# Kernel tuning notes

Measured on AMD Instinct MI355X. Metric: run time of the kernel, lower is better.

Reference implementation:

```python
import jax, jax.numpy as jnp
import numpy as np

T = 4096
C = 2048
N_FEAT = 2048
NEG = -1e30  # finite stand-in for -inf so fully-masked (padding) rows stay NaN-free


def setup_inputs() -> dict:
    key = jax.random.key(0)
    kx, kw, kb = jax.random.split(key, 3)
    x = jax.random.normal(kx, (T, C), dtype=jnp.float32)
    # Dense(features=3*n_feat): kernel (C, 3*n_feat), bias (3*n_feat,)
    W = jax.random.normal(kw, (C, 3 * N_FEAT), dtype=jnp.float32) * (1.0 / np.sqrt(C))
    b = jax.random.normal(kb, (3 * N_FEAT,), dtype=jnp.float32) * 0.01
    n_padd = 128
    return {"x": x, "W": W, "b": b, "n_padd": n_padd}


def reference(x, W, b, n_padd):
    T_, _ = x.shape
    qkv = x @ W + b                      # (T, 3*n_feat)
    q, k, v = jnp.split(qkv, 3, axis=1)  # each (T, n_feat)
    scale = 1.0 / jnp.sqrt(jnp.float32(q.shape[1]))
    att = (q @ k.T) * scale              # (T, T)
    rows = jnp.arange(T_)[:, None]
    cols = jnp.arange(T_)[None, :]
    # causal AND both row/col past the left padding
    mask = (cols <= rows) & (cols >= n_padd) & (rows >= n_padd)
    att = jnp.where(mask, att, NEG)
    p = jax.nn.softmax(att, axis=1)      # stable row softmax
    # kernel only stores rows >= n_padd; padding rows are zero
    p = jnp.where(rows >= n_padd, p, 0.0)
    y = p @ v                            # (T, n_feat)
    return y
```

## Files before the change

kernel.cpp:

```cpp
#include <hip/hip_runtime.h>
#include <cstdint>


#define T_DIM 4096
#define C_DIM 2048
#define NF    2048
#define N3    6144
#define NEGV  (-1e30f)

typedef __bf16 bf16x8 __attribute__((ext_vector_type(8)));
typedef __bf16 bf16x4 __attribute__((ext_vector_type(4)));
typedef float  f32x4  __attribute__((ext_vector_type(4)));

#define FENCE() asm volatile("" ::: "memory")
#define BARRIER() do { FENCE(); __builtin_amdgcn_s_barrier(); FENCE(); } while (0)

__device__ __forceinline__ void async_cp16(const void* g, void* l) {
    __builtin_amdgcn_global_load_lds(
        reinterpret_cast<const __attribute__((address_space(1))) unsigned int*>(
            reinterpret_cast<uintptr_t>(g)),
        reinterpret_cast<__attribute__((address_space(3))) unsigned int*>(
            reinterpret_cast<uintptr_t>(l)),
        16, 0, 0);
}

__device__ __forceinline__ void gemm_loop(const __bf16* A, const __bf16* B,
                                          int lda, int ldb, int m0, int n0,
                                          int kiters, __bf16* As, __bf16* Bs,
                                          f32x4 (&acc)[4][4]) {
    if (kiters <= 0) return;
    const int t    = threadIdx.x;
    const int wv   = t >> 6;
    const int lane = t & 63;
    const int srow = t >> 3;
    const int scol = (((t & 7) ^ (srow & 7)) << 3);
    const int wm   = (wv >> 1) << 6;
    const int wn   = (wv & 1) << 6;
    const int lrow = lane & 15;
    const int kq   = lane >> 4;
    const int swz  = lrow & 7;
    const int rc0  = ((kq ^ swz) << 3);
    const int rc1  = (((kq | 4) ^ swz) << 3);

    const __bf16* ga = A + (size_t)(m0 + srow) * lda + scol;
    const __bf16* gb = B + (size_t)(n0 + srow) * ldb + scol;

    auto stage = [&](int kk, int s) {
#pragma unroll
        for (int i = 0; i < 4; ++i) {
            async_cp16(ga + kk * 64 + (size_t)(32 * i) * lda,
                       &As[s * 8192 + i * 2048 + wv * 512]);
            async_cp16(gb + kk * 64 + (size_t)(32 * i) * ldb,
                       &Bs[s * 8192 + i * 2048 + wv * 512]);
        }
    };
    auto loadF = [&](const __bf16* Ab, const __bf16* Bb, int rc,
                     bf16x8 (&af)[4], bf16x8 (&bfr)[4]) {
#pragma unroll
        for (int mi = 0; mi < 4; ++mi)
            af[mi] = *(const bf16x8*)&Ab[(wm + mi * 16 + lrow) * 64 + rc];
#pragma unroll
        for (int ni = 0; ni < 4; ++ni)
            bfr[ni] = *(const bf16x8*)&Bb[(wn + ni * 16 + lrow) * 64 + rc];
    };
    auto mfma16 = [&](bf16x8 (&af)[4], bf16x8 (&bfr)[4]) {
        __builtin_amdgcn_s_setprio(1);
#pragma unroll
        for (int mi = 0; mi < 4; ++mi)
#pragma unroll
            for (int ni = 0; ni < 4; ++ni)
                acc[mi][ni] = __builtin_amdgcn_mfma_f32_16x16x32_bf16(
                    af[mi], bfr[ni], acc[mi][ni], 0, 0, 0);
        __builtin_amdgcn_s_setprio(0);
    };

    bf16x8 af[4], bfr[4];

    stage(0, 0);
    asm volatile("s_waitcnt vmcnt(0)" ::: "memory");
    BARRIER();

    for (int kk = 0; kk < kiters; ++kk) {
        const int b = kk & 1;
        const __bf16* Ab = &As[b * 8192];
        const __bf16* Bb = &Bs[b * 8192];
        const bool pf = (kk + 1 < kiters);
        if (pf) stage(kk + 1, b ^ 1);
        loadF(Ab, Bb, rc0, af, bfr);
        mfma16(af, bfr);
        loadF(Ab, Bb, rc1, af, bfr);
        mfma16(af, bfr);
        asm volatile("s_waitcnt vmcnt(0)" ::: "memory");
        BARRIER();
    }
}

__global__ void prep_kernel(const float* __restrict__ x,
                            __bf16* __restrict__ xb,
                            const float* __restrict__ W,
                            __bf16* __restrict__ Wt) {
    if (blockIdx.x < 2048) {
        const int n4 = (T_DIM * C_DIM) / 4;
        const int stride = 2048 * 256;
        for (int i = blockIdx.x * 256 + threadIdx.x; i < n4; i += stride) {
            float4 v = ((const float4*)x)[i];
            bf16x4 o;
            o[0] = (__bf16)v.x; o[1] = (__bf16)v.y;
            o[2] = (__bf16)v.z; o[3] = (__bf16)v.w;
            ((bf16x4*)xb)[i] = o;
        }
        return;
    }
    __shared__ float tile[32][33];
    const int tb = blockIdx.x - 2048;
    const int bx = (tb % (N3 / 32)) * 32;
    const int by = (tb / (N3 / 32)) * 32;
    const int tx = threadIdx.x & 31, ty = threadIdx.x >> 5;
#pragma unroll
    for (int i = 0; i < 32; i += 8)
        tile[ty + i][tx] = W[(size_t)(by + ty + i) * N3 + bx + tx];
    __syncthreads();
#pragma unroll
    for (int i = 0; i < 32; i += 8)
        Wt[(size_t)(bx + ty + i) * C_DIM + by + tx] = (__bf16)tile[tx][ty + i];
}

#define EPILOG_SETUP()                                     \
    const int t = threadIdx.x, wv = t >> 6, lane = t & 63; \
    const int wm = (wv >> 1) << 6, wn = (wv & 1) << 6;     \
    const int rq = (lane >> 4) << 2, cn = lane & 15

__global__ void __launch_bounds__(768)
qkv_gemm_kernel(const __bf16* __restrict__ xb, const __bf16* __restrict__ Wt,
                const float* __restrict__ bias, __bf16* __restrict__ qb,
                __bf16* __restrict__ kb, __bf16* __restrict__ vT) {
    __shared__ __bf16 As[2][256 * 64];
    __shared__ __bf16 Bs[2][384 * 64];

    const int t    = threadIdx.x;
    const int wv   = t >> 6;
    const int lane = t & 63;
    const int srow = t >> 3;
    const int scol = (((t & 7) ^ (srow & 7)) << 3);
    const int m0   = blockIdx.x * 256;
    const int n0   = blockIdx.y * 384;
    const int wmo  = (wv / 6) * 128;
    const int wno  = (wv % 6) * 64;
    const int lrow = lane & 15;
    const int kq   = lane >> 4;
    const int swz  = lrow & 7;
    const int rc0  = ((kq ^ swz) << 3);
    const int rc1  = (((kq | 4) ^ swz) << 3);

    const __bf16* ga = xb + (size_t)(m0 + srow) * C_DIM + scol;
    const __bf16* gb = Wt + (size_t)(n0 + srow) * C_DIM + scol;

    f32x4 acc[8][4] = {};

    auto stageA = [&](int kt, int s) {
        const __bf16* a = ga + kt * 64;
        async_cp16(a, &As[s][wv * 512]);
        async_cp16(a + (size_t)96 * C_DIM, &As[s][6144 + wv * 512]);
        if (wv < 8)
            async_cp16(a + (size_t)192 * C_DIM, &As[s][12288 + wv * 512]);
    };
    auto stageB2 = [&](int kt, int s, int h) {
        const __bf16* b2 = gb + kt * 64 + (size_t)(192 * h) * C_DIM;
        async_cp16(b2, &Bs[s][h * 12288 + wv * 512]);
        async_cp16(b2 + (size_t)96 * C_DIM, &Bs[s][h * 12288 + 6144 + wv * 512]);
    };
    auto loadA4 = [&](const __bf16* Ab, int mh, int rc, bf16x8 (&af)[4]) {
#pragma unroll
        for (int mi = 0; mi < 4; ++mi)
            af[mi] = *(const bf16x8*)
                &Ab[(wmo + mh * 64 + mi * 16 + lrow) * 64 + rc];
    };
    auto loadB4 = [&](const __bf16* Bb, int rc, bf16x8 (&bfr)[4]) {
#pragma unroll
        for (int ni = 0; ni < 4; ++ni)
            bfr[ni] = *(const bf16x8*)&Bb[(wno + ni * 16 + lrow) * 64 + rc];
    };
    auto mfma16 = [&](bf16x8 (&af)[4], bf16x8 (&bfr)[4], int mh) {
        __builtin_amdgcn_s_setprio(1);
#pragma unroll
        for (int mi = 0; mi < 4; ++mi)
#pragma unroll
            for (int ni = 0; ni < 4; ++ni)
                acc[mh * 4 + mi][ni] = __builtin_amdgcn_mfma_f32_16x16x32_bf16(
                    af[mi], bfr[ni], acc[mh * 4 + mi][ni], 0, 0, 0);
        __builtin_amdgcn_s_setprio(0);
    };

    bf16x8 af[4], bfr[4];
    constexpr int KT = C_DIM / 64;

    stageA(0, 0); stageB2(0, 0, 0); stageB2(0, 0, 1);
    asm volatile("s_waitcnt vmcnt(0)" ::: "memory");
    BARRIER();

    for (int kt = 0; kt < KT; ++kt) {
        const int b = kt & 1;
        const __bf16* Ab = As[b];
        const __bf16* Bb = Bs[b];
        const bool pf = (kt + 1 < KT);
        loadB4(Bb, rc0, bfr);
        loadA4(Ab, 0, rc0, af);
        if (pf) stageA(kt + 1, b ^ 1);
        BARRIER();
        mfma16(af, bfr, 0);
        BARRIER();
        loadA4(Ab, 1, rc0, af);
        if (pf) stageB2(kt + 1, b ^ 1, 0);
        BARRIER();
        mfma16(af, bfr, 1);
        BARRIER();
        loadB4(Bb, rc1, bfr);
        loadA4(Ab, 0, rc1, af);
        if (pf) stageB2(kt + 1, b ^ 1, 1);
        BARRIER();
        mfma16(af, bfr, 0);
        BARRIER();
        loadA4(Ab, 1, rc1, af);
        BARRIER();
        mfma16(af, bfr, 1);
        if (pf) asm volatile("s_waitcnt vmcnt(0)" ::: "memory");
        BARRIER();
    }

    const int rq = (lane >> 4) << 2, cn = lane & 15;
#pragma unroll
    for (int mi = 0; mi < 8; ++mi)
#pragma unroll
        for (int ni = 0; ni < 4; ++ni) {
            int col = n0 + wno + ni * 16 + cn;
            float bv = bias[col];
            if (col >= 2 * NF) {
                bf16x4 o;
#pragma unroll
                for (int r = 0; r < 4; ++r) o[r] = (__bf16)(acc[mi][ni][r] + bv);
                int row = m0 + wmo + mi * 16 + rq;
                *(bf16x4*)&vT[(size_t)(col - 2 * NF) * T_DIM + row] = o;
            } else {
#pragma unroll
                for (int r = 0; r < 4; ++r) {
                    int row = m0 + wmo + mi * 16 + rq + r;
                    float val = acc[mi][ni][r] + bv;
                    if (col < NF)
                        qb[(size_t)row * NF + col] = (__bf16)val;
                    else
                        kb[(size_t)row * NF + (col - NF)] = (__bf16)val;
                }
            }
        }
}

__global__ void __launch_bounds__(256)
sc_gemm_kernel(const __bf16* __restrict__ qb, const __bf16* __restrict__ kb,
               __bf16* __restrict__ S, const int* __restrict__ npadd_p) {
    int i = blockIdx.x;
    int mt = (int)((sqrtf(8.0f * (float)i + 1.0f) - 1.0f) * 0.5f);
    while ((mt + 1) * (mt + 2) / 2 <= i) ++mt;
    while (mt * (mt + 1) / 2 > i) --mt;
    int nt = i - mt * (mt + 1) / 2;
    const int m0 = mt * 128, n0 = nt * 128;
    const int npadd = *npadd_p;
    if (m0 + 128 <= npadd || n0 + 128 <= npadd) return;

    __shared__ __bf16 As[2 * 128 * 64];
    __shared__ __bf16 Bs[2 * 128 * 64];
    f32x4 acc[4][4] = {};
    gemm_loop(qb, kb, NF, NF, m0, n0, NF / 64, As, Bs, acc);

    const float scale = 0.022097086912079608f;
    EPILOG_SETUP();
#pragma unroll
    for (int mi = 0; mi < 4; ++mi)
#pragma unroll
        for (int ni = 0; ni < 4; ++ni) {
            int j = n0 + wn + ni * 16 + cn;
#pragma unroll
            for (int r = 0; r < 4; ++r) {
                int row = m0 + wm + mi * 16 + rq + r;
                S[(size_t)row * T_DIM + j] = (__bf16)(acc[mi][ni][r] * scale);
            }
        }
}

__global__ void __launch_bounds__(256)
softmax_kernel(const __bf16* __restrict__ S, __bf16* __restrict__ P,
               const int* __restrict__ npadd_p) {
    const int wv = threadIdx.x >> 6, lane = threadIdx.x & 63;
    const int row = blockIdx.x * 4 + wv;
    const int npadd = *npadd_p;
    __bf16* prow = P + (size_t)row * T_DIM;

    if (row < npadd) {
        bf16x8 z = {};
#pragma unroll
        for (int c = 0; c < 8; ++c) ((bf16x8*)prow)[c * 64 + lane] = z;
        return;
    }

    const __bf16* srow = S + (size_t)row * T_DIM;
    float vals[64];
    float mx = NEGV;
#pragma unroll
    for (int c = 0; c < 8; ++c) {
        if (c * 512 > row) {
#pragma unroll
            for (int e = 0; e < 8; ++e) vals[c * 8 + e] = NEGV;
            continue;
        }
        int j0 = c * 512 + lane * 8;
        bf16x8 v = ((const bf16x8*)srow)[c * 64 + lane];
#pragma unroll
        for (int e = 0; e < 8; ++e) {
            float f = (j0 + e >= npadd && j0 + e <= row) ? (float)v[e] : NEGV;
            vals[c * 8 + e] = f;
            mx = fmaxf(mx, f);
        }
    }
#pragma unroll
    for (int o = 32; o > 0; o >>= 1) mx = fmaxf(mx, __shfl_xor(mx, o));

    float sm = 0.f;
#pragma unroll
    for (int k = 0; k < 64; ++k) {
        vals[k] = exp2f((vals[k] - mx) * 1.4426950408889634f);
        sm += vals[k];
    }
#pragma unroll
    for (int o = 32; o > 0; o >>= 1) sm += __shfl_xor(sm, o);
    float inv = 1.0f / sm;

#pragma unroll
    for (int c = 0; c < 8; ++c) {
        bf16x8 o;
#pragma unroll
        for (int e = 0; e < 8; ++e) o[e] = (__bf16)(vals[c * 8 + e] * inv);
        ((bf16x8*)prow)[c * 64 + lane] = o;
    }
}

__global__ void __launch_bounds__(256)
pv_gemm_kernel(const __bf16* __restrict__ P, const __bf16* __restrict__ vT,
               float* __restrict__ out, const int* __restrict__ npadd_p) {
    const int idx = blockIdx.x;
    const int kskip = *npadd_p >> 6;
    int mt, nt, start, iters;
    bool atomic_out;
    if (idx < 256) {
        mt = idx & 15; nt = idx >> 4;
        int kt = (mt + 1) * 2 - kskip; if (kt < 0) kt = 0;
        start = kskip; iters = kt; atomic_out = false;
    } else {
        int j = idx - 256;
        mt = 16 + (j & 15); nt = (j >> 4) & 15;
        int half = j >> 8;
        int kt = (mt + 1) * 2 - kskip; if (kt < 0) kt = 0;
        int h0 = (kt + 1) >> 1;
        start = kskip + (half ? h0 : 0);
        iters = half ? kt - h0 : h0;
        atomic_out = true;
    }
    const int m0 = mt * 128, n0 = nt * 128;

    __shared__ __bf16 As[2 * 128 * 64];
    __shared__ __bf16 Bs[2 * 128 * 64];
    f32x4 acc[4][4] = {};
    gemm_loop(P + (size_t)start * 64, vT + (size_t)start * 64,
              T_DIM, T_DIM, m0, n0, iters, As, Bs, acc);

    EPILOG_SETUP();
#pragma unroll
    for (int mi = 0; mi < 4; ++mi)
#pragma unroll
        for (int ni = 0; ni < 4; ++ni) {
            int col = n0 + wn + ni * 16 + cn;
#pragma unroll
            for (int r = 0; r < 4; ++r) {
                int row = m0 + wm + mi * 16 + rq + r;
                float* p = &out[(size_t)row * NF + col];
                if (atomic_out) unsafeAtomicAdd(p, acc[mi][ni][r]);
                else            *p = acc[mi][ni][r];
            }
        }
}

extern "C" void kernel_launch(void* const* d_in, const int* in_sizes, int n_in,
                              void* d_out, int out_size, void* d_ws,
                              size_t ws_size, hipStream_t stream) {
    const float* x = (const float*)d_in[0];
    const float* W = (const float*)d_in[1];
    const float* b = (const float*)d_in[2];
    const int* npadd = (const int*)d_in[3];
    float* out = (float*)d_out;

    char* ws = (char*)d_ws;
    __bf16* xb = (__bf16*)(ws);
    __bf16* Wt = (__bf16*)(ws + (16ull << 20));
    __bf16* qb = (__bf16*)(ws + (40ull << 20));
    __bf16* kb = (__bf16*)(ws + (56ull << 20));
    __bf16* vT = (__bf16*)(ws + (72ull << 20));
    __bf16* S  = (__bf16*)(ws + (88ull << 20));
    __bf16* P  = (__bf16*)(ws + (40ull << 20));

    hipMemsetAsync(out + (size_t)2048 * NF, 0, (size_t)2048 * NF * 4, stream);

    prep_kernel<<<2048 + (N3 / 32) * (C_DIM / 32), 256, 0, stream>>>(x, xb, W, Wt);
    qkv_gemm_kernel<<<dim3(T_DIM / 256, N3 / 384), 768, 0, stream>>>(xb, Wt, b,
                                                                     qb, kb, vT);
    sc_gemm_kernel<<<528, 256, 0, stream>>>(qb, kb, S, npadd);
    softmax_kernel<<<T_DIM / 4, 256, 0, stream>>>(S, P, npadd);
    pv_gemm_kernel<<<768, 256, 0, stream>>>(P, vT, out, npadd);
}
```

Before: 385.8 us.

## Rework QKV GEMM to 256x256 tiles with register double-buffered pipeline

The QKV projection GEMM changes from 256x384 tiles with 12 waves to 256x256 tiles with 8 waves, moved into a reusable gemm256 helper. The main loop drops most of the per-phase barriers, keeping one per k-step, and double-buffers the fragment registers so LDS reads for the next sub-step are issued while MFMAs run. The next k-slab fragments are also preloaded after the barrier. The epilogue picks the q/k/v destination per block instead of per element. The grid grows from 16x16 to 16x24 blocks; fewer barriers means better overlap, at the cost of higher register pressure and a different tile-count balance across CUs.

```diff
diff --git a/kernel.cpp b/kernel.cpp
--- a/kernel.cpp
+++ b/kernel.cpp
@@ -95,6 +95,103 @@
     }
 }
 
+__device__ __forceinline__ void gemm256(const __bf16* A, const __bf16* B,
+                                        int lda, int ldb, int m0, int n0,
+                                        int kiters, __bf16* As, __bf16* Bs,
+                                        f32x4 (&acc)[8][4]) {
+    if (kiters <= 0) return;
+    const int t    = threadIdx.x;
+    const int wv   = t >> 6;
+    const int lane = t & 63;
+    const int srow = t >> 3;
+    const int scol = (((t & 7) ^ (srow & 7)) << 3);
+    const int wmo  = (wv >> 2) * 128;
+    const int wno  = (wv & 3) * 64;
+    const int lrow = lane & 15;
+    const int kq   = lane >> 4;
+    const int swz  = lrow & 7;
+    const int rc0  = ((kq ^ swz) << 3);
+    const int rc1  = (((kq | 4) ^ swz) << 3);
+
+    const __bf16* ga = A + (size_t)(m0 + srow) * lda + scol;
+    const __bf16* gb = B + (size_t)(n0 + srow) * ldb + scol;
+
+    auto stA4 = [&](int kk, int s) {
+        const __bf16* a = ga + kk * 64;
+        __bf16* dst = As + s * 16384 + wv * 512;
+#pragma unroll
+        for (int j = 0; j < 4; ++j)
+            async_cp16(a + (size_t)(64 * j) * lda, dst + j * 4096);
+    };
+    auto stB4 = [&](int kk, int s) {
+        const __bf16* b2 = gb + kk * 64;
+        __bf16* dst = Bs + s * 16384 + wv * 512;
+#pragma unroll
+        for (int j = 0; j < 4; ++j)
+            async_cp16(b2 + (size_t)(64 * j) * ldb, dst + j * 4096);
+    };
+    auto loadA4 = [&](const __bf16* Ab, int mh, int rc, bf16x8 (&af)[4]) {
+#pragma unroll
+        for (int mi = 0; mi < 4; ++mi)
+            af[mi] = *(const bf16x8*)
+                &Ab[(wmo + mh * 64 + mi * 16 + lrow) * 64 + rc];
+    };
+    auto loadB4 = [&](const __bf16* Bb, int rc, bf16x8 (&bfr)[4]) {
+#pragma unroll
+        for (int ni = 0; ni < 4; ++ni)
+            bfr[ni] = *(const bf16x8*)&Bb[(wno + ni * 16 + lrow) * 64 + rc];
+    };
+    auto mfma16 = [&](bf16x8 (&af)[4], bf16x8 (&bfr)[4], int mh) {
+        __builtin_amdgcn_s_setprio(1);
+#pragma unroll
+        for (int mi = 0; mi < 4; ++mi)
+#pragma unroll
+            for (int ni = 0; ni < 4; ++ni)
+                acc[mh * 4 + mi][ni] = __builtin_amdgcn_mfma_f32_16x16x32_bf16(
+                    af[mi], bfr[ni], acc[mh * 4 + mi][ni], 0, 0, 0);
+        __builtin_amdgcn_s_setprio(0);
+    };
+
+    bf16x8 afA[4], afB[4], bfrA[4], bfrB[4];
+
+    stA4(0, 0); stB4(0, 0);
+    asm volatile("s_waitcnt vmcnt(0)" ::: "memory");
+    BARRIER();
+    loadB4(Bs, rc0, bfrA);
+    loadA4(As, 0, rc0, afA);
+
+    for (int kt = 0; kt < kiters; ++kt) {
+        const int b = kt & 1;
+        const __bf16* Ab = As + b * 16384;
+        const __bf16* Bb = Bs + b * 16384;
+        const bool pf = (kt + 1 < kiters);
+        if (pf) { stA4(kt + 1, b ^ 1); stB4(kt + 1, b ^ 1); }
+        loadA4(Ab, 1, rc0, afB);
+        mfma16(afA, bfrA, 0);
+        loadB4(Bb, rc1, bfrB);
+        loadA4(Ab, 0, rc1, afA);
+        mfma16(afB, bfrA, 1);
+        loadA4(Ab, 1, rc1, afB);
+        mfma16(afA, bfrB, 0);
+        mfma16(afB, bfrB, 1);
+        asm volatile("s_waitcnt vmcnt(0)" ::: "memory");
+        BARRIER();
+        if (pf) {
+            loadB4(Bs + (b ^ 1) * 16384, rc0, bfrA);
+            loadA4(As + (b ^ 1) * 16384, 0, rc0, afA);
+        }
+    }
+}
+
+#define EPILOG_SETUP()                                     \
+    const int t = threadIdx.x, wv = t >> 6, lane = t & 63; \
+    const int wm = (wv >> 1) << 6, wn = (wv & 1) << 6;     \
+    const int rq = (lane >> 4) << 2, cn = lane & 15
+#define EPI256()                                            \
+    const int t = threadIdx.x, wv = t >> 6, lane = t & 63;  \
+    const int wmo = (wv >> 2) * 128, wno = (wv & 3) * 64;   \
+    const int rq = (lane >> 4) << 2, cn = lane & 15
+
 __global__ void prep_kernel(const float* __restrict__ x,
                             __bf16* __restrict__ xb,
                             const float* __restrict__ W,
@@ -125,133 +222,49 @@
         Wt[(size_t)(bx + ty + i) * C_DIM + by + tx] = (__bf16)tile[tx][ty + i];
 }
 
-#define EPILOG_SETUP()                                     \
-    const int t = threadIdx.x, wv = t >> 6, lane = t & 63; \
-    const int wm = (wv >> 1) << 6, wn = (wv & 1) << 6;     \
-    const int rq = (lane >> 4) << 2, cn = lane & 15
-
-__global__ void __launch_bounds__(768)
+__global__ void __launch_bounds__(512)
 qkv_gemm_kernel(const __bf16* __restrict__ xb, const __bf16* __restrict__ Wt,
                 const float* __restrict__ bias, __bf16* __restrict__ qb,
                 __bf16* __restrict__ kb, __bf16* __restrict__ vT) {
-    __shared__ __bf16 As[2][256 * 64];
-    __shared__ __bf16 Bs[2][384 * 64];
-
-    const int t    = threadIdx.x;
-    const int wv   = t >> 6;
-    const int lane = t & 63;
-    const int srow = t >> 3;
-    const int scol = (((t & 7) ^ (srow & 7)) << 3);
-    const int m0   = blockIdx.x * 256;
-    const int n0   = blockIdx.y * 384;
-    const int wmo  = (wv / 6) * 128;
-    const int wno  = (wv % 6) * 64;
-    const int lrow = lane & 15;
-    const int kq   = lane >> 4;
-    const int swz  = lrow & 7;
-    const int rc0  = ((kq ^ swz) << 3);
-    const int rc1  = (((kq | 4) ^ swz) << 3);
-
-    const __bf16* ga = xb + (size_t)(m0 + srow) * C_DIM + scol;
-    const __bf16* gb = Wt + (size_t)(n0 + srow) * C_DIM + scol;
-
+    __shared__ __bf16 As[2 * 256 * 64];
+    __shared__ __bf16 Bs[2 * 256 * 64];
     f32x4 acc[8][4] = {};
-
-    auto stageA = [&](int kt, int s) {
-        const __bf16* a = ga + kt * 64;
-        async_cp16(a, &As[s][wv * 512]);
-        async_cp16(a + (size_t)96 * C_DIM, &As[s][6144 + wv * 512]);
-        if (wv < 8)
-            async_cp16(a + (size_t)192 * C_DIM, &As[s][12288 + wv * 512]);
-    };
-    auto stageB2 = [&](int kt, int s, int h) {
-        const __bf16* b2 = gb + kt * 64 + (size_t)(192 * h) * C_DIM;
-        async_cp16(b2, &Bs[s][h * 12288 + wv * 512]);
-        async_cp16(b2 + (size_t)96 * C_DIM, &Bs[s][h * 12288 + 6144 + wv * 512]);
-    };
-    auto loadA4 = [&](const __bf16* Ab, int mh, int rc, bf16x8 (&af)[4]) {
-#pragma unroll
-        for (int mi = 0; mi < 4; ++mi)
-            af[mi] = *(const bf16x8*)
-                &Ab[(wmo + mh * 64 + mi * 16 + lrow) * 64 + rc];
-    };
-    auto loadB4 = [&](const __bf16* Bb, int rc, bf16x8 (&bfr)[4]) {
-#pragma unroll
-        for (int ni = 0; ni < 4; ++ni)
-            bfr[ni] = *(const bf16x8*)&Bb[(wno + ni * 16 + lrow) * 64 + rc];
-    };
-    auto mfma16 = [&](bf16x8 (&af)[4], bf16x8 (&bfr)[4], int mh) {
-        __builtin_amdgcn_s_setprio(1);
-#pragma unroll
-        for (int mi = 0; mi < 4; ++mi)
-#pragma unroll
-            for (int ni = 0; ni < 4; ++ni)
-                acc[mh * 4 + mi][ni] = __builtin_amdgcn_mfma_f32_16x16x32_bf16(
-                    af[mi], bfr[ni], acc[mh * 4 + mi][ni], 0, 0, 0);
-        __builtin_amdgcn_s_setprio(0);
-    };
-
-    bf16x8 af[4], bfr[4];
-    constexpr int KT = C_DIM / 64;
-
-    stageA(0, 0); stageB2(0, 0, 0); stageB2(0, 0, 1);
-    asm volatile("s_waitcnt vmcnt(0)" ::: "memory");
-    BARRIER();
-
-    for (int kt = 0; kt < KT; ++kt) {
-        const int b = kt & 1;
-        const __bf16* Ab = As[b];
-        const __bf16* Bb = Bs[b];
-        const bool pf = (kt + 1 < KT);
-        loadB4(Bb, rc0, bfr);
-        loadA4(Ab, 0, rc0, af);
-        if (pf) stageA(kt + 1, b ^ 1);
-        BARRIER();
-        mfma16(af, bfr, 0);
-        BARRIER();
-        loadA4(Ab, 1, rc0, af);
-        if (pf) stageB2(kt + 1, b ^ 1, 0);
-        BARRIER();
-        mfma16(af, bfr, 1);
-        BARRIER();
-        loadB4(Bb, rc1, bfr);
-        loadA4(Ab, 0, rc1, af);
-        if (pf) stageB2(kt + 1, b ^ 1, 1);
-        BARRIER();
-        mfma16(af, bfr, 0);
-        BARRIER();
-        loadA4(Ab, 1, rc1, af);
-        BARRIER();
-        mfma16(af, bfr, 1);
-        if (pf) asm volatile("s_waitcnt vmcnt(0)" ::: "memory");
-        BARRIER();
-    }
-
-    const int rq = (lane >> 4) << 2, cn = lane & 15;
-#pragma unroll
-    for (int mi = 0; mi < 8; ++mi)
-#pragma unroll
-        for (int ni = 0; ni < 4; ++ni) {
-            int col = n0 + wno + ni * 16 + cn;
-            float bv = bias[col];
-            if (col >= 2 * NF) {
+    const int m0 = blockIdx.x * 256;
+    const int by = blockIdx.y;
+    const int n0 = by * 256;
+    gemm256(xb, Wt, C_DIM, C_DIM, m0, n0, C_DIM / 64, As, Bs, acc);
+
+    EPI256();
+    if (by >= 16) {
+#pragma unroll
+        for (int mi = 0; mi < 8; ++mi)
+#pragma unroll
+            for (int ni = 0; ni < 4; ++ni) {
+                int col = n0 + wno + ni * 16 + cn;
+                float bv = bias[col];
                 bf16x4 o;
 #pragma unroll
                 for (int r = 0; r < 4; ++r) o[r] = (__bf16)(acc[mi][ni][r] + bv);
                 int row = m0 + wmo + mi * 16 + rq;
                 *(bf16x4*)&vT[(size_t)(col - 2 * NF) * T_DIM + row] = o;
-            } else {
+            }
+    } else {
+        __bf16* dst = (by < 8) ? qb : kb;
+        const int coff = (by < 8) ? 0 : NF;
+#pragma unroll
+        for (int mi = 0; mi < 8; ++mi)
+#pragma unroll
+            for (int ni = 0; ni < 4; ++ni) {
+                int col = n0 + wno + ni * 16 + cn;
+                float bv = bias[col];
 #pragma unroll
                 for (int r = 0; r < 4; ++r) {
                     int row = m0 + wmo + mi * 16 + rq + r;
-                    float val = acc[mi][ni][r] + bv;
-                    if (col < NF)
-                        qb[(size_t)row * NF + col] = (__bf16)val;
-                    else
-                        kb[(size_t)row * NF + (col - NF)] = (__bf16)val;
+                    dst[(size_t)row * NF + (col - coff)] =
+                        (__bf16)(acc[mi][ni][r] + bv);
                 }
             }
-        }
+    }
 }
 
 __global__ void __launch_bounds__(256)
@@ -408,7 +421,7 @@
     hipMemsetAsync(out + (size_t)2048 * NF, 0, (size_t)2048 * NF * 4, stream);
 
     prep_kernel<<<2048 + (N3 / 32) * (C_DIM / 32), 256, 0, stream>>>(x, xb, W, Wt);
-    qkv_gemm_kernel<<<dim3(T_DIM / 256, N3 / 384), 768, 0, stream>>>(xb, Wt, b,
+    qkv_gemm_kernel<<<dim3(T_DIM / 256, N3 / 256), 512, 0, stream>>>(xb, Wt, b,
                                                                      qb, kb, vT);
     sc_gemm_kernel<<<528, 256, 0, stream>>>(qb, kb, S, npadd);
     softmax_kernel<<<T_DIM / 4, 256, 0, stream>>>(S, P, npadd);
```

Result: faster. 349.9 us (-9.3%).
